# Kernel optimization log

Measured on AMD Instinct MI355X. Metric: run time of the kernel, lower is better.

## Reference

```python
import jax, jax.numpy as jnp
import numpy as np

B, N, DIM, HEADS, DHEAD, DEPTH, EDGE = 1, 384, 128, 4, 64, 3, 8
INNER = HEADS * DHEAD  # 256


def _make_rotary():
    inv = 1.0 / (10000.0 ** (np.arange(0, DHEAD, 2, dtype=np.float32) / DHEAD))
    f = np.arange(N, dtype=np.float32)[:, None] * inv[None, :]  # [N, DHEAD//2]
    f = np.repeat(f, 2, axis=-1)  # interleaved pairs -> [N, DHEAD]
    return jnp.asarray(np.cos(f)), jnp.asarray(np.sin(f))

COS, SIN = _make_rotary()


def _rotate_half(x):
    x2 = x.reshape(x.shape[:-1] + (DHEAD // 2, 2))
    return jnp.stack((-x2[..., 1], x2[..., 0]), axis=-1).reshape(x.shape)


def _layer_norm(x, s, b, eps=1e-3):
    mu = jnp.mean(x, axis=-1, keepdims=True)
    var = jnp.mean(jnp.square(x - mu), axis=-1, keepdims=True)
    return (x - mu) * jax.lax.rsqrt(var + eps) * s + b


def _gated_res(x, res, Wg):
    gi = jnp.concatenate([x, res, x - res], axis=-1)  # [B,N,3*DIM]
    g = jax.nn.sigmoid(gi @ Wg)  # [B,N,1]
    return x * g + res * (1.0 - g)


def setup_inputs() -> dict:
    key = jax.random.key(0)
    ks = jax.random.split(key, 16)
    p = lambda k, shape: 0.02 * jax.random.normal(k, shape, jnp.float32)
    return {
        "nodes": jax.random.normal(ks[0], (B, N, DIM), jnp.float32),
        "edges": jax.random.normal(ks[1], (B, N, N, EDGE), jnp.float32),
        "ln1_s": jnp.ones((DEPTH, DIM), jnp.float32), "ln1_b": jnp.zeros((DEPTH, DIM), jnp.float32),
        "Wq": p(ks[2], (DEPTH, DIM, INNER)), "bq": jnp.zeros((DEPTH, INNER), jnp.float32),
        "Wkv": p(ks[3], (DEPTH, DIM, 2 * INNER)), "bkv": jnp.zeros((DEPTH, 2 * INNER), jnp.float32),
        "We": p(ks[4], (DEPTH, EDGE, INNER)), "be": jnp.zeros((DEPTH, INNER), jnp.float32),
        "Wo": p(ks[5], (DEPTH, INNER, DIM)), "bo": jnp.zeros((DEPTH, DIM), jnp.float32),
        "Wg_attn": p(ks[6], (DEPTH, 3 * DIM, 1)),
        "ln2_s": jnp.ones((DEPTH, DIM), jnp.float32), "ln2_b": jnp.zeros((DEPTH, DIM), jnp.float32),
        "W1": p(ks[7], (DEPTH, DIM, 4 * DIM)), "b1": jnp.zeros((DEPTH, 4 * DIM), jnp.float32),
        "W2": p(ks[8], (DEPTH, 4 * DIM, DIM)), "b2": jnp.zeros((DEPTH, DIM), jnp.float32),
        "Wg_ff": p(ks[9], (DEPTH, 3 * DIM, 1)),
        "Wd1": p(ks[10], (DIM, 9)), "bd1": jnp.zeros((9,), jnp.float32),
        "Wd2": p(ks[11], (9, 3)), "bd2": jnp.zeros((3,), jnp.float32),
        "mask": jnp.ones((B, N), dtype=bool),
    }


def _forward(nodes, edges, ln1_s, ln1_b, Wq, bq, Wkv, bkv, We, be, Wo, bo, Wg_attn,
             ln2_s, ln2_b, W1, b1, W2, b2, Wg_ff, Wd1, bd1, Wd2, bd2, mask):
    cos = COS[None, None]  # [1,1,N,DHEAD]
    sin = SIN[None, None]
    mask2 = mask[:, None, :, None] & mask[:, None, None, :]  # [B,1,N,N]
    x = nodes
    for i in range(DEPTH):
        # --- pre-norm attention with edge-conditioned K/V and rotary pos emb ---
        xn = _layer_norm(x, ln1_s[i], ln1_b[i])
        q = (xn @ Wq[i] + bq[i]).reshape(B, N, HEADS, DHEAD).transpose(0, 2, 1, 3)
        k, v = jnp.split(xn @ Wkv[i] + bkv[i], 2, axis=-1)
        k = k.reshape(B, N, HEADS, DHEAD).transpose(0, 2, 1, 3)
        v = v.reshape(B, N, HEADS, DHEAD).transpose(0, 2, 1, 3)
        e = (edges @ We[i] + be[i]).reshape(B, N, N, HEADS, DHEAD).transpose(0, 3, 1, 2, 4)  # [B,H,i,j,d]
        q = q * cos + _rotate_half(q) * sin
        k = k * cos + _rotate_half(k) * sin
        kf = k[:, :, None, :, :] + e  # [B,H,i,j,d]
        vf = v[:, :, None, :, :] + e
        sim = jnp.einsum('bhid,bhijd->bhij', q, kf) * (DHEAD ** -0.5)
        sim = jnp.where(mask2, sim, -1e9)
        attn = jax.nn.softmax(sim, axis=-1)
        out = jnp.einsum('bhij,bhijd->bhid', attn, vf)
        out = out.transpose(0, 2, 1, 3).reshape(B, N, INNER) @ Wo[i] + bo[i]
        x = _gated_res(out, x, Wg_attn[i])
        # --- pre-norm feedforward ---
        xn2 = _layer_norm(x, ln2_s[i], ln2_b[i])
        h = jax.nn.gelu(xn2 @ W1[i] + b1[i], approximate=False)
        ff = h @ W2[i] + b2[i]
        x = _gated_res(ff, x, Wg_ff[i])
    y = jax.nn.relu(x @ Wd1 + bd1)
    y = y @ Wd2 + bd2  # [B,N,3]
    return y - jnp.mean(y, axis=1)  # broadcasts since B == 1 (matches TF semantics)


def reference(nodes, edges, ln1_s, ln1_b, Wq, bq, Wkv, bkv, We, be, Wo, bo, Wg_attn,
              ln2_s, ln2_b, W1, b1, W2, b2, Wg_ff, Wd1, bd1, Wd2, bd2, mask):
    return _forward(nodes, edges, ln1_s, ln1_b, Wq, bq, Wkv, bkv, We, be, Wo, bo, Wg_attn,
                    ln2_s, ln2_b, W1, b1, W2, b2, Wg_ff, Wd1, bd1, Wd2, bd2, mask)
```

## Files before the change

kernel.cpp:

```cpp
#include <hip/hip_runtime.h>
#include <math.h>

#define NTOK 384
#define DIM  128
#define HEADS 4
#define DHEAD 64
#define INNER 256
#define DEPTH 3
#define EDGE 8
#define FFD 512

__device__ __forceinline__ float wave_sum64(float v){
#pragma unroll
  for (int m = 32; m >= 1; m >>= 1) v += __shfl_xor(v, m, 64);
  return v;
}
__device__ __forceinline__ float wave_max64(float v){
#pragma unroll
  for (int m = 32; m >= 1; m >>= 1) v = fmaxf(v, __shfl_xor(v, m, 64));
  return v;
}

__device__ __forceinline__ int swz_row(int id){ return (id & 7) * 48 + (id >> 3); }

__device__ __forceinline__ void rotary_val(int i, int d, float* c, float* s){
  int j = d >> 1;
  double ex = (double)(2 * j) / 64.0;
  float p = (float)pow(10000.0, ex);
  float inv = 1.0f / p;
  float f = (float)i * inv;
  double fd = (double)f;
  *c = (float)cos(fd);
  *s = (float)sin(fd);
}

__device__ __forceinline__ void qkv_row_512(
    int i, int t, const float* __restrict__ snx,
    const float* __restrict__ Wq, const float* __restrict__ bq,
    const float* __restrict__ Wkv, const float* __restrict__ bkv,
    const float* __restrict__ We, const float* __restrict__ be,
    const float* __restrict__ cosRow, const float* __restrict__ sinRow,
    float* __restrict__ qb_, float* __restrict__ kbT, float* __restrict__ vb_,
    float* __restrict__ qWeB, float* __restrict__ qbeB)
{
  if (t >= 384) return;
  const float2* Wp; const float* bb; int pcol; int stride;
  if (t < 128)      { Wp = (const float2*)Wq + t;              stride = 128; bb = bq;        pcol = t; }
  else if (t < 256) { Wp = (const float2*)Wkv + (t - 128);     stride = 256; bb = bkv;       pcol = t - 128; }
  else              { Wp = (const float2*)Wkv + 128 + (t - 256); stride = 256; bb = bkv + 256; pcol = t - 256; }

  float a0 = 0.f, a1 = 0.f;
#pragma unroll 8
  for (int k = 0; k < 128; ++k){
    float2 w = Wp[(size_t)k * stride];
    float xr = snx[k];
    a0 = fmaf(xr, w.x, a0); a1 = fmaf(xr, w.y, a1);
  }
  a0 += bb[2 * pcol]; a1 += bb[2 * pcol + 1];

  if (t < 256){
    int dloc = (2 * pcol) & 63;
    float c = cosRow[dloc], s = sinRow[dloc];
    float r0 = a0 * c - a1 * s;
    float r1 = a1 * c + a0 * s;
    if (t < 128){
      qb_[i * 256 + 2 * pcol]     = r0;
      qb_[i * 256 + 2 * pcol + 1] = r1;
      int h = pcol >> 5;
#pragma unroll
      for (int cc = 0; cc < 8; ++cc){
        float pr = r0 * We[cc * 256 + 2 * pcol] + r1 * We[cc * 256 + 2 * pcol + 1];
#pragma unroll
        for (int m = 16; m >= 1; m >>= 1) pr += __shfl_xor(pr, m, 32);
        if ((t & 31) == 0) qWeB[(h * NTOK + i) * 8 + cc] = pr;
      }
      float pb = r0 * be[2 * pcol] + r1 * be[2 * pcol + 1];
#pragma unroll
      for (int m = 16; m >= 1; m >>= 1) pb += __shfl_xor(pb, m, 32);
      if ((t & 31) == 0) qbeB[h * NTOK + i] = pb;
    } else {
      int h = pcol >> 5, d0 = 2 * (pcol & 31);
      kbT[(size_t)(h * 64 + d0) * NTOK + i]     = r0;
      kbT[(size_t)(h * 64 + d0 + 1) * NTOK + i] = r1;
    }
  } else {
    vb_[i * 256 + 2 * pcol]     = a0;
    vb_[i * 256 + 2 * pcol + 1] = a1;
  }
}

__global__ __launch_bounds__(512) void k_lnqkv(
    const float* __restrict__ x,
    const float* __restrict__ ls, const float* __restrict__ lb,
    const float* __restrict__ Wq, const float* __restrict__ bq,
    const float* __restrict__ Wkv, const float* __restrict__ bkv,
    const float* __restrict__ We, const float* __restrict__ be,
    float* __restrict__ cosS, float* __restrict__ sinS,
    float* __restrict__ qb_, float* __restrict__ kbT, float* __restrict__ vb_,
    float* __restrict__ qWeB, float* __restrict__ qbeB)
{
  __shared__ float snx[128];
  __shared__ float crow[64], srow[64];
  __shared__ float red[4];
  int i = swz_row(blockIdx.x);
  int t = threadIdx.x;

  if (t >= 448){
    int d = t - 448;
    float c, s;
    rotary_val(i, d, &c, &s);
    crow[d] = c; srow[d] = s;
    cosS[i * 64 + d] = c; sinS[i * 64 + d] = s;
  }
  float xv = (t < 128) ? x[(size_t)i * 128 + t] : 0.f;
  float s = (t < 128) ? wave_sum64(xv) : 0.f;
  if (t == 0)  red[0] = s;
  if (t == 64) red[1] = s;
  __syncthreads();
  float mu = (red[0] + red[1]) * (1.0f / 128.0f);
  float d = xv - mu;
  float s2 = (t < 128) ? wave_sum64(d * d) : 0.f;
  if (t == 0)  red[2] = s2;
  if (t == 64) red[3] = s2;
  __syncthreads();
  if (t < 128){
    float var = (red[2] + red[3]) * (1.0f / 128.0f);
    float rstd = 1.0f / sqrtf(var + 1e-3f);
    snx[t] = d * rstd * ls[t] + lb[t];
  }
  __syncthreads();
  qkv_row_512(i, t, snx, Wq, bq, Wkv, bkv, We, be, crow, srow,
              qb_, kbT, vb_, qWeB, qbeB);
}

__global__ __launch_bounds__(384) void k_attn(
    const float* __restrict__ qb_, const float* __restrict__ kbT, const float* __restrict__ vb_,
    const float* __restrict__ qWeB, const float* __restrict__ qbeB,
    const float* __restrict__ edges,
    const float* __restrict__ We, const float* __restrict__ be,
    float* __restrict__ aout)
{
  __shared__ float qs[64];
  __shared__ float qw[8];
  __shared__ float qbs_s;
  __shared__ float attnL[NTOK];
  __shared__ float redA[6], redB[6];
  __shared__ float red8[6][8];
  __shared__ float aws[8];
  __shared__ float part[NTOK];

  int id = blockIdx.x;
  int xcd = id & 7, loc = id >> 3;
  int i = xcd * 48 + (loc % 48);
  int h = loc / 48;
  int t = threadIdx.x, lane = t & 63, wv = t >> 6;

  if (t < 64) qs[t] = qb_[i * 256 + h * 64 + t];
  else if (t < 72) qw[t - 64] = qWeB[(h * NTOK + i) * 8 + (t - 64)];
  else if (t == 72) qbs_s = qbeB[h * NTOK + i];
  __syncthreads();

  const float* kTp = kbT + (size_t)(h * 64) * NTOK + t;
  float ac0 = 0.f, ac1 = 0.f, ac2 = 0.f, ac3 = 0.f;
#pragma unroll 8
  for (int d = 0; d < 64; d += 4){
    ac0 = fmaf(qs[d],     kTp[(size_t)d * NTOK],       ac0);
    ac1 = fmaf(qs[d + 1], kTp[(size_t)(d + 1) * NTOK], ac1);
    ac2 = fmaf(qs[d + 2], kTp[(size_t)(d + 2) * NTOK], ac2);
    ac3 = fmaf(qs[d + 3], kTp[(size_t)(d + 3) * NTOK], ac3);
  }
  const float* ep = edges + ((size_t)i * NTOK + t) * 8;
  float4 e0 = *(const float4*)ep;
  float4 e1 = *(const float4*)(ep + 4);
  float ed = e0.x * qw[0] + e0.y * qw[1] + e0.z * qw[2] + e0.w * qw[3]
           + e1.x * qw[4] + e1.y * qw[5] + e1.z * qw[6] + e1.w * qw[7];
  float sim = 0.125f * (ac0 + ac1 + ac2 + ac3 + ed + qbs_s);

  float mx = wave_max64(sim);
  if (lane == 0) redA[wv] = mx;
  __syncthreads();
  float gm = fmaxf(fmaxf(fmaxf(redA[0], redA[1]), fmaxf(redA[2], redA[3])),
                   fmaxf(redA[4], redA[5]));
  float e = expf(sim - gm);
  float sm = wave_sum64(e);
  if (lane == 0) redB[wv] = sm;
  __syncthreads();
  float tot = redB[0] + redB[1] + redB[2] + redB[3] + redB[4] + redB[5];
  float w = e / tot;
  attnL[t] = w;

  float a8[8] = { w * e0.x, w * e0.y, w * e0.z, w * e0.w,
                  w * e1.x, w * e1.y, w * e1.z, w * e1.w };
#pragma unroll
  for (int cc = 0; cc < 8; ++cc){
    float r = wave_sum64(a8[cc]);
    if (lane == 0) red8[wv][cc] = r;
  }
  __syncthreads();
  if (t < 8){
    float sa = 0.f;
#pragma unroll
    for (int g = 0; g < 6; ++g) sa += red8[g][t];
    aws[t] = sa;
  }
  __syncthreads();

  {
    int dd = lane;
    const float* vp = vb_ + h * 64 + dd;
    int j0 = wv * 64;
    float va = 0.f, vb2 = 0.f;
#pragma unroll 8
    for (int jj = 0; jj < 64; jj += 2){
      va  = fmaf(attnL[j0 + jj],     vp[(size_t)(j0 + jj) * 256],     va);
      vb2 = fmaf(attnL[j0 + jj + 1], vp[(size_t)(j0 + jj + 1) * 256], vb2);
    }
    part[t] = va + vb2;
  }
  __syncthreads();
  if (t < 64){
    float o = part[t] + part[64 + t] + part[128 + t] + part[192 + t]
            + part[256 + t] + part[320 + t];
    float ew = 0.f;
#pragma unroll
    for (int cc = 0; cc < 8; ++cc) ew = fmaf(aws[cc], We[cc * 256 + h * 64 + t], ew);
    o += ew + be[h * 64 + t];
    aout[i * 256 + h * 64 + t] = o;
  }
}

__global__ __launch_bounds__(512) void k_tail(
    const float* __restrict__ aout,
    const float* __restrict__ Wo, const float* __restrict__ bo,
    const float* __restrict__ Wg_a,
    const float* __restrict__ ln2s, const float* __restrict__ ln2b,
    const float* __restrict__ W1, const float* __restrict__ b1,
    const float* __restrict__ W2, const float* __restrict__ b2,
    const float* __restrict__ Wg_f,
    const float* __restrict__ xin, float* __restrict__ xout,
    int has_next,
    const float* __restrict__ ls_n, const float* __restrict__ lb_n,
    const float* __restrict__ Wq_n, const float* __restrict__ bq_n,
    const float* __restrict__ Wkv_n, const float* __restrict__ bkv_n,
    const float* __restrict__ We_n, const float* __restrict__ be_n,
    const float* __restrict__ cosS, const float* __restrict__ sinS,
    float* __restrict__ qb_, float* __restrict__ kbT, float* __restrict__ vb_,
    float* __restrict__ qWeB, float* __restrict__ qbeB)
{
  __shared__ float ar[256];
  __shared__ float xold[128];
  __shared__ float xrow[128];
  __shared__ float snx[128];
  __shared__ float hs[512];
  __shared__ float4 prL[512];
  __shared__ float red[4];
  float* prF = (float*)prL;

  int i = swz_row(blockIdx.x);
  int t = threadIdx.x;

  if (t < 64)            ((float4*)ar)[t]        = ((const float4*)(aout + (size_t)i * 256))[t];
  else if (t < 96)       ((float4*)xold)[t - 64] = ((const float4*)(xin + (size_t)i * 128))[t - 64];
  __syncthreads();

  {
    int colq = t & 31, ksub = t >> 5;
    const float4* Wo4 = (const float4*)Wo;
    float4 acc = {0.f, 0.f, 0.f, 0.f};
#pragma unroll
    for (int kk = 0; kk < 16; ++kk){
      int k = ksub * 16 + kk;
      float4 w = Wo4[(size_t)k * 32 + colq];
      float a = ar[k];
      acc.x = fmaf(a, w.x, acc.x); acc.y = fmaf(a, w.y, acc.y);
      acc.z = fmaf(a, w.z, acc.z); acc.w = fmaf(a, w.w, acc.w);
    }
    prL[ksub * 32 + colq] = acc;
  }
  __syncthreads();

  float o = 0.f;
  if (t < 128){
    o = bo[t];
#pragma unroll
    for (int s = 0; s < 16; ++s) o += prF[s * 128 + t];
    float xo = xold[t];
    float gp = o * Wg_a[t] + xo * Wg_a[128 + t] + (o - xo) * Wg_a[256 + t];
    float sg = wave_sum64(gp);
    if (t == 0)  red[0] = sg;
    if (t == 64) red[1] = sg;
  }
  __syncthreads();
  if (t < 128){
    float z = red[0] + red[1];
    float gg = 1.0f / (1.0f + expf(-z));
    xrow[t] = o * gg + xold[t] * (1.0f - gg);
  }
  __syncthreads();
  float xv2 = (t < 128) ? xrow[t] : 0.f;
  float s = (t < 128) ? wave_sum64(xv2) : 0.f;
  if (t == 0)  red[0] = s;
  if (t == 64) red[1] = s;
  __syncthreads();
  float mu = (red[0] + red[1]) * (1.0f / 128.0f);
  float dcen = xv2 - mu;
  float s2 = (t < 128) ? wave_sum64(dcen * dcen) : 0.f;
  if (t == 0)  red[2] = s2;
  if (t == 64) red[3] = s2;
  __syncthreads();
  if (t < 128){
    float var = (red[2] + red[3]) * (1.0f / 128.0f);
    float rstd = 1.0f / sqrtf(var + 1e-3f);
    snx[t] = dcen * rstd * ln2s[t] + ln2b[t];
  }
  __syncthreads();

  {
    int colq = t & 127, ksub = t >> 7;
    const float4* W14 = (const float4*)W1;
    float4 acc = {0.f, 0.f, 0.f, 0.f};
#pragma unroll 8
    for (int kk = 0; kk < 32; ++kk){
      int k = ksub * 32 + kk;
      float4 w = W14[(size_t)k * 128 + colq];
      float a = snx[k];
      acc.x = fmaf(a, w.x, acc.x); acc.y = fmaf(a, w.y, acc.y);
      acc.z = fmaf(a, w.z, acc.z); acc.w = fmaf(a, w.w, acc.w);
    }
    prL[ksub * 128 + colq] = acc;
  }
  __syncthreads();

  {
    float h = b1[t];
#pragma unroll
    for (int s3 = 0; s3 < 4; ++s3) h += prF[s3 * 512 + t];
    const float RS2 = 0.70710678118654752440f;
    hs[t] = 0.5f * h * (1.0f + erff(h * RS2));
  }
  __syncthreads();

  {
    int colq = t & 31, ksub = t >> 5;
    const float4* W24 = (const float4*)W2;
    float4 acc = {0.f, 0.f, 0.f, 0.f};
#pragma unroll 8
    for (int kk = 0; kk < 32; ++kk){
      int k = ksub * 32 + kk;
      float4 w = W24[(size_t)k * 32 + colq];
      float a = hs[k];
      acc.x = fmaf(a, w.x, acc.x); acc.y = fmaf(a, w.y, acc.y);
      acc.z = fmaf(a, w.z, acc.z); acc.w = fmaf(a, w.w, acc.w);
    }
    prL[ksub * 32 + colq] = acc;
  }
  __syncthreads();

  float f = 0.f;
  if (t < 128){
    f = b2[t];
#pragma unroll
    for (int s3 = 0; s3 < 16; ++s3) f += prF[s3 * 128 + t];
    float xr = xrow[t];
    float gp = f * Wg_f[t] + xr * Wg_f[128 + t] + (f - xr) * Wg_f[256 + t];
    float sg = wave_sum64(gp);
    if (t == 0)  red[0] = sg;
    if (t == 64) red[1] = sg;
  }
  __syncthreads();
  float xnew = 0.f;
  if (t < 128){
    float z = red[0] + red[1];
    float gg = 1.0f / (1.0f + expf(-z));
    xnew = f * gg + xrow[t] * (1.0f - gg);
    xout[(size_t)i * 128 + t] = xnew;
  }
  if (has_next){
    float sn = (t < 128) ? wave_sum64(xnew) : 0.f;
    if (t == 0)  red[0] = sn;
    if (t == 64) red[1] = sn;
    __syncthreads();
    float mun = (red[0] + red[1]) * (1.0f / 128.0f);
    float dn = xnew - mun;
    float sn2 = (t < 128) ? wave_sum64(dn * dn) : 0.f;
    if (t == 0)  red[2] = sn2;
    if (t == 64) red[3] = sn2;
    __syncthreads();
    if (t < 128){
      float var = (red[2] + red[3]) * (1.0f / 128.0f);
      float rstd = 1.0f / sqrtf(var + 1e-3f);
      snx[t] = dn * rstd * ls_n[t] + lb_n[t];
    }
    __syncthreads();
    qkv_row_512(i, t, snx, Wq_n, bq_n, Wkv_n, bkv_n, We_n, be_n,
                cosS + (size_t)i * 64, sinS + (size_t)i * 64,
                qb_, kbT, vb_, qWeB, qbeB);
  }
}

__global__ __launch_bounds__(384) void k_final(
    const float* __restrict__ x,
    const float* __restrict__ Wd1, const float* __restrict__ bd1,
    const float* __restrict__ Wd2, const float* __restrict__ bd2,
    float* __restrict__ out)
{
  __shared__ float red[6];
  int i = threadIdx.x;
  float y[9];
#pragma unroll
  for (int c = 0; c < 9; ++c) y[c] = bd1[c];
  const float4* x4 = (const float4*)(x + (size_t)i * 128);
#pragma unroll 8
  for (int r4 = 0; r4 < 32; ++r4){
    float4 xv = x4[r4];
    const float* wp = Wd1 + (r4 * 4) * 9;
#pragma unroll
    for (int c = 0; c < 9; ++c) y[c] = fmaf(xv.x, wp[c], y[c]);
#pragma unroll
    for (int c = 0; c < 9; ++c) y[c] = fmaf(xv.y, wp[9 + c], y[c]);
#pragma unroll
    for (int c = 0; c < 9; ++c) y[c] = fmaf(xv.z, wp[18 + c], y[c]);
#pragma unroll
    for (int c = 0; c < 9; ++c) y[c] = fmaf(xv.w, wp[27 + c], y[c]);
  }
#pragma unroll
  for (int c = 0; c < 9; ++c) y[c] = fmaxf(y[c], 0.0f);
  float z[3];
#pragma unroll
  for (int c = 0; c < 3; ++c){
    float a = bd2[c];
#pragma unroll
    for (int r = 0; r < 9; ++r) a = fmaf(y[r], Wd2[r * 3 + c], a);
    z[c] = a;
  }
#pragma unroll
  for (int c = 0; c < 3; ++c){
    float s = wave_sum64(z[c]);
    if ((i & 63) == 0) red[i >> 6] = s;
    __syncthreads();
    float tot = 0.f;
#pragma unroll
    for (int w = 0; w < 6; ++w) tot += red[w];
    float mean = tot * (1.0f / 384.0f);
    out[i * 3 + c] = z[c] - mean;
    __syncthreads();
  }
}

extern "C" void kernel_launch(void* const* d_in, const int* in_sizes, int n_in,
                              void* d_out, int out_size, void* d_ws, size_t ws_size,
                              hipStream_t stream)
{
  const float* nodes   = (const float*)d_in[0];
  const float* edges   = (const float*)d_in[1];
  const float* ln1_s   = (const float*)d_in[2];
  const float* ln1_b   = (const float*)d_in[3];
  const float* Wq      = (const float*)d_in[4];
  const float* bq      = (const float*)d_in[5];
  const float* Wkv     = (const float*)d_in[6];
  const float* bkv     = (const float*)d_in[7];
  const float* We      = (const float*)d_in[8];
  const float* be      = (const float*)d_in[9];
  const float* Wo      = (const float*)d_in[10];
  const float* bo      = (const float*)d_in[11];
  const float* Wg_attn = (const float*)d_in[12];
  const float* ln2_s   = (const float*)d_in[13];
  const float* ln2_b   = (const float*)d_in[14];
  const float* W1      = (const float*)d_in[15];
  const float* b1      = (const float*)d_in[16];
  const float* W2      = (const float*)d_in[17];
  const float* b2      = (const float*)d_in[18];
  const float* Wg_ff   = (const float*)d_in[19];
  const float* Wd1     = (const float*)d_in[20];
  const float* bd1     = (const float*)d_in[21];
  const float* Wd2     = (const float*)d_in[22];
  const float* bd2     = (const float*)d_in[23];

  float* ws   = (float*)d_ws;
  float* cosS = ws;
  float* sinS = cosS + 24576;
  float* qbuf = sinS + 24576;
  float* kbT  = qbuf + 98304;
  float* vbuf = kbT + 98304;
  float* qWeB = vbuf + 98304;
  float* qbeB = qWeB + 12288;
  float* aoutB = qbeB + 1536;
  float* xbuf = aoutB + 98304;

  k_lnqkv<<<dim3(NTOK), dim3(512), 0, stream>>>(
      nodes, ln1_s, ln1_b, Wq, bq, Wkv, bkv, We, be,
      cosS, sinS, qbuf, kbT, vbuf, qWeB, qbeB);

  for (int L = 0; L < DEPTH; ++L){
    int Ln = (L < DEPTH - 1) ? (L + 1) : L;
    k_attn<<<dim3(NTOK * HEADS), dim3(384), 0, stream>>>(
        qbuf, kbT, vbuf, qWeB, qbeB, edges,
        We + (size_t)L * EDGE * INNER, be + L * INNER, aoutB);
    k_tail<<<dim3(NTOK), dim3(512), 0, stream>>>(
        aoutB, Wo + (size_t)L * INNER * DIM, bo + L * DIM,
        Wg_attn + L * 3 * DIM,
        ln2_s + L * DIM, ln2_b + L * DIM,
        W1 + (size_t)L * DIM * FFD, b1 + L * FFD,
        W2 + (size_t)L * FFD * DIM, b2 + L * DIM,
        Wg_ff + L * 3 * DIM,
        (L == 0) ? nodes : xbuf, xbuf,
        (L < DEPTH - 1) ? 1 : 0,
        ln1_s + Ln * DIM, ln1_b + Ln * DIM,
        Wq + (size_t)Ln * DIM * INNER, bq + Ln * INNER,
        Wkv + (size_t)Ln * DIM * 2 * INNER, bkv + Ln * 2 * INNER,
        We + (size_t)Ln * EDGE * INNER, be + Ln * INNER,
        cosS, sinS, qbuf, kbT, vbuf, qWeB, qbeB);
  }

  k_final<<<dim3(1), dim3(384), 0, stream>>>(xbuf, Wd1, bd1, Wd2, bd2, (float*)d_out);
}
```

Measured before the change: 153.9 us.

## Split fused tail kernel into projection, FFN and QKV kernels with more blocks

Replaces the single per-row tail kernel, which ran one 512-thread block per token, with four smaller kernels: output projection plus gate plus LN2, FFN1 split over two column halves, FFN2 split over two column halves, and the next layer's QKV split into three parts. The aim is to raise the block count and parallelism so more CUs are busy during the serial per-row GEMVs. The cost is extra launches and global round trips for intermediate buffers. The gate and layernorm work is also recomputed in each of the three QKV blocks.

```diff
diff --git a/kernel.cpp b/kernel.cpp
--- a/kernel.cpp
+++ b/kernel.cpp
@@ -229,63 +229,202 @@
   }
 }
 
-__global__ __launch_bounds__(512) void k_tail(
+__global__ __launch_bounds__(256) void k_projgate(
     const float* __restrict__ aout,
     const float* __restrict__ Wo, const float* __restrict__ bo,
     const float* __restrict__ Wg_a,
     const float* __restrict__ ln2s, const float* __restrict__ ln2b,
+    const float* __restrict__ xin,
+    float* __restrict__ snx2buf, float* __restrict__ xrowB)
+{
+  __shared__ float ain[256];
+  __shared__ float xo[128];
+  __shared__ float orow[128];
+  __shared__ float xrow[128];
+  __shared__ float4 pr[256];
+  __shared__ float red[4];
+
+  int i = swz_row(blockIdx.x);
+  int t = threadIdx.x;
+
+  ain[t] = aout[(size_t)i * 256 + t];
+  if (t < 128) xo[t] = xin[(size_t)i * 128 + t];
+  __syncthreads();
+
+  {
+    int cq = t & 31, ks = t >> 5;
+    const float4* Wo4 = (const float4*)Wo;
+    float4 acc = {0.f, 0.f, 0.f, 0.f};
+#pragma unroll
+    for (int kk = 0; kk < 32; ++kk){
+      int k = ks * 32 + kk;
+      float4 w = Wo4[(size_t)k * 32 + cq];
+      float a = ain[k];
+      acc.x = fmaf(a, w.x, acc.x); acc.y = fmaf(a, w.y, acc.y);
+      acc.z = fmaf(a, w.z, acc.z); acc.w = fmaf(a, w.w, acc.w);
+    }
+    pr[ks * 32 + cq] = acc;
+  }
+  __syncthreads();
+  if (t < 32){
+    float4 s = pr[t];
+#pragma unroll
+    for (int s3 = 1; s3 < 8; ++s3){
+      float4 p = pr[s3 * 32 + t];
+      s.x += p.x; s.y += p.y; s.z += p.z; s.w += p.w;
+    }
+    float4 b = ((const float4*)bo)[t];
+    s.x += b.x; s.y += b.y; s.z += b.z; s.w += b.w;
+    ((float4*)orow)[t] = s;
+  }
+  __syncthreads();
+
+  if (t < 128){
+    float o = orow[t], xov = xo[t];
+    float gp = o * Wg_a[t] + xov * Wg_a[128 + t] + (o - xov) * Wg_a[256 + t];
+    float sg = wave_sum64(gp);
+    if (t == 0)  red[0] = sg;
+    if (t == 64) red[1] = sg;
+  }
+  __syncthreads();
+  if (t < 128){
+    float z = red[0] + red[1];
+    float gg = 1.0f / (1.0f + expf(-z));
+    float xr = orow[t] * gg + xo[t] * (1.0f - gg);
+    xrow[t] = xr;
+    xrowB[(size_t)i * 128 + t] = xr;
+    float s = wave_sum64(xr);
+    if (t == 0)  red[2] = s;
+    if (t == 64) red[3] = s;
+  }
+  __syncthreads();
+  if (t < 128){
+    float mu = (red[2] + red[3]) * (1.0f / 128.0f);
+    float dc = xrow[t] - mu;
+    float s2 = wave_sum64(dc * dc);
+    if (t == 0)  red[0] = s2;
+    if (t == 64) red[1] = s2;
+    __syncthreads();
+    float var = (red[0] + red[1]) * (1.0f / 128.0f);
+    float rstd = 1.0f / sqrtf(var + 1e-3f);
+    snx2buf[(size_t)i * 128 + t] = dc * rstd * ln2s[t] + ln2b[t];
+  } else {
+    __syncthreads();
+  }
+}
+
+__global__ __launch_bounds__(256) void k_ffn1(
+    const float* __restrict__ snx2buf,
     const float* __restrict__ W1, const float* __restrict__ b1,
+    float* __restrict__ hbuf)
+{
+  __shared__ float sx[128];
+  __shared__ float2 pr2[128];
+  int id = blockIdx.x;
+  int xcd = id & 7, loc = id >> 3;
+  int i = xcd * 48 + (loc >> 1);
+  int ch = loc & 1;
+  int t = threadIdx.x;
+
+  if (t < 128) sx[t] = snx2buf[(size_t)i * 128 + t];
+  __syncthreads();
+
+  int cp = t & 127, ks = t >> 7;
+  int c2 = ch * 128 + cp;
+  const float2* W12 = (const float2*)W1;
+  float a0 = 0.f, a1 = 0.f;
+#pragma unroll 8
+  for (int kk = 0; kk < 64; ++kk){
+    int k = ks * 64 + kk;
+    float2 w = W12[(size_t)k * 256 + c2];
+    float x = sx[k];
+    a0 = fmaf(x, w.x, a0); a1 = fmaf(x, w.y, a1);
+  }
+  if (ks == 1){ pr2[cp].x = a0; pr2[cp].y = a1; }
+  __syncthreads();
+  if (ks == 0){
+    a0 += pr2[cp].x + b1[2 * c2];
+    a1 += pr2[cp].y + b1[2 * c2 + 1];
+    const float RS2 = 0.70710678118654752440f;
+    float g0 = 0.5f * a0 * (1.0f + erff(a0 * RS2));
+    float g1 = 0.5f * a1 * (1.0f + erff(a1 * RS2));
+    float2 gv; gv.x = g0; gv.y = g1;
+    ((float2*)hbuf)[(size_t)i * 256 + c2] = gv;
+  }
+}
+
+__global__ __launch_bounds__(256) void k_ffn2(
+    const float* __restrict__ hbuf,
     const float* __restrict__ W2, const float* __restrict__ b2,
+    float* __restrict__ fbuf)
+{
+  __shared__ float hh[512];
+  __shared__ float4 pr[256];
+  int id = blockIdx.x;
+  int xcd = id & 7, loc = id >> 3;
+  int i = xcd * 48 + (loc >> 1);
+  int hc = loc & 1;
+  int t = threadIdx.x;
+
+  hh[t] = hbuf[(size_t)i * 512 + t];
+  hh[256 + t] = hbuf[(size_t)i * 512 + 256 + t];
+  __syncthreads();
+
+  int q = t & 15, ks = t >> 4;
+  int gq = hc * 16 + q;
+  const float4* W24 = (const float4*)W2;
+  float4 acc = {0.f, 0.f, 0.f, 0.f};
+#pragma unroll
+  for (int kk = 0; kk < 32; ++kk){
+    int k = ks * 32 + kk;
+    float4 w = W24[(size_t)k * 32 + gq];
+    float a = hh[k];
+    acc.x = fmaf(a, w.x, acc.x); acc.y = fmaf(a, w.y, acc.y);
+    acc.z = fmaf(a, w.z, acc.z); acc.w = fmaf(a, w.w, acc.w);
+  }
+  pr[ks * 16 + q] = acc;
+  __syncthreads();
+  if (t < 16){
+    float4 s = pr[t];
+#pragma unroll
+    for (int s3 = 1; s3 < 16; ++s3){
+      float4 p = pr[s3 * 16 + t];
+      s.x += p.x; s.y += p.y; s.z += p.z; s.w += p.w;
+    }
+    float4 b = ((const float4*)b2)[gq];
+    s.x += b.x; s.y += b.y; s.z += b.z; s.w += b.w;
+    ((float4*)fbuf)[(size_t)i * 32 + gq] = s;
+  }
+}
+
+__global__ __launch_bounds__(256) void k_qkv(
+    const float* __restrict__ fbuf, const float* __restrict__ xrowB,
     const float* __restrict__ Wg_f,
-    const float* __restrict__ xin, float* __restrict__ xout,
-    int has_next,
     const float* __restrict__ ls_n, const float* __restrict__ lb_n,
     const float* __restrict__ Wq_n, const float* __restrict__ bq_n,
     const float* __restrict__ Wkv_n, const float* __restrict__ bkv_n,
     const float* __restrict__ We_n, const float* __restrict__ be_n,
     const float* __restrict__ cosS, const float* __restrict__ sinS,
+    float* __restrict__ xbuf,
     float* __restrict__ qb_, float* __restrict__ kbT, float* __restrict__ vb_,
     float* __restrict__ qWeB, float* __restrict__ qbeB)
 {
-  __shared__ float ar[256];
-  __shared__ float xold[128];
-  __shared__ float xrow[128];
   __shared__ float snx[128];
-  __shared__ float hs[512];
-  __shared__ float4 prL[512];
+  __shared__ float xnewL[128];
+  __shared__ float2 qp2[128];
   __shared__ float red[4];
-  float* prF = (float*)prL;
-
-  int i = swz_row(blockIdx.x);
+
+  int id = blockIdx.x;
+  int xcd = id & 7, loc = id >> 3;
+  int i = xcd * 48 + loc / 3;
+  int part = loc % 3;
   int t = threadIdx.x;
 
-  if (t < 64)            ((float4*)ar)[t]        = ((const float4*)(aout + (size_t)i * 256))[t];
-  else if (t < 96)       ((float4*)xold)[t - 64] = ((const float4*)(xin + (size_t)i * 128))[t - 64];
-  __syncthreads();
-
-  {
-    int colq = t & 31, ksub = t >> 5;
-    const float4* Wo4 = (const float4*)Wo;
-    float4 acc = {0.f, 0.f, 0.f, 0.f};
-#pragma unroll
-    for (int kk = 0; kk < 16; ++kk){
-      int k = ksub * 16 + kk;
-      float4 w = Wo4[(size_t)k * 32 + colq];
-      float a = ar[k];
-      acc.x = fmaf(a, w.x, acc.x); acc.y = fmaf(a, w.y, acc.y);
-      acc.z = fmaf(a, w.z, acc.z); acc.w = fmaf(a, w.w, acc.w);
-    }
-    prL[ksub * 32 + colq] = acc;
-  }
-  __syncthreads();
-
-  float o = 0.f;
+  float fv = 0.f, xr = 0.f;
   if (t < 128){
-    o = bo[t];
-#pragma unroll
-    for (int s = 0; s < 16; ++s) o += prF[s * 128 + t];
-    float xo = xold[t];
-    float gp = o * Wg_a[t] + xo * Wg_a[128 + t] + (o - xo) * Wg_a[256 + t];
+    fv = fbuf[(size_t)i * 128 + t];
+    xr = xrowB[(size_t)i * 128 + t];
+    float gp = fv * Wg_f[t] + xr * Wg_f[128 + t] + (fv - xr) * Wg_f[256 + t];
     float sg = wave_sum64(gp);
     if (t == 0)  red[0] = sg;
     if (t == 64) red[1] = sg;
@@ -294,108 +433,97 @@
   if (t < 128){
     float z = red[0] + red[1];
     float gg = 1.0f / (1.0f + expf(-z));
-    xrow[t] = o * gg + xold[t] * (1.0f - gg);
-  }
-  __syncthreads();
-  float xv2 = (t < 128) ? xrow[t] : 0.f;
-  float s = (t < 128) ? wave_sum64(xv2) : 0.f;
-  if (t == 0)  red[0] = s;
-  if (t == 64) red[1] = s;
-  __syncthreads();
-  float mu = (red[0] + red[1]) * (1.0f / 128.0f);
-  float dcen = xv2 - mu;
-  float s2 = (t < 128) ? wave_sum64(dcen * dcen) : 0.f;
-  if (t == 0)  red[2] = s2;
-  if (t == 64) red[3] = s2;
+    float xn = fv * gg + xr * (1.0f - gg);
+    xnewL[t] = xn;
+    if (part == 0) xbuf[(size_t)i * 128 + t] = xn;
+    float s = wave_sum64(xn);
+    if (t == 0)  red[2] = s;
+    if (t == 64) red[3] = s;
+  }
   __syncthreads();
   if (t < 128){
-    float var = (red[2] + red[3]) * (1.0f / 128.0f);
+    float mu = (red[2] + red[3]) * (1.0f / 128.0f);
+    float dn = xnewL[t] - mu;
+    float s2 = wave_sum64(dn * dn);
+    if (t == 0)  red[0] = s2;
+    if (t == 64) red[1] = s2;
+    __syncthreads();
+    float var = (red[0] + red[1]) * (1.0f / 128.0f);
     float rstd = 1.0f / sqrtf(var + 1e-3f);
-    snx[t] = dcen * rstd * ln2s[t] + ln2b[t];
-  }
-  __syncthreads();
-
-  {
-    int colq = t & 127, ksub = t >> 7;
-    const float4* W14 = (const float4*)W1;
-    float4 acc = {0.f, 0.f, 0.f, 0.f};
+    snx[t] = dn * rstd * ls_n[t] + lb_n[t];
+  } else {
+    __syncthreads();
+  }
+  __syncthreads();
+
+  int cp = t & 127, ks = t >> 7;
+  const float2* Wp; const float* bb; int stride;
+  if (part == 0)      { Wp = (const float2*)Wq_n + cp;        stride = 128; bb = bq_n; }
+  else if (part == 1) { Wp = (const float2*)Wkv_n + cp;       stride = 256; bb = bkv_n; }
+  else                { Wp = (const float2*)Wkv_n + 128 + cp; stride = 256; bb = bkv_n + 256; }
+
+  float a0 = 0.f, a1 = 0.f;
 #pragma unroll 8
-    for (int kk = 0; kk < 32; ++kk){
-      int k = ksub * 32 + kk;
-      float4 w = W14[(size_t)k * 128 + colq];
-      float a = snx[k];
-      acc.x = fmaf(a, w.x, acc.x); acc.y = fmaf(a, w.y, acc.y);
-      acc.z = fmaf(a, w.z, acc.z); acc.w = fmaf(a, w.w, acc.w);
+  for (int kk = 0; kk < 64; ++kk){
+    int k = ks * 64 + kk;
+    float2 w = Wp[(size_t)k * stride];
+    float x = snx[k];
+    a0 = fmaf(x, w.x, a0); a1 = fmaf(x, w.y, a1);
+  }
+  if (ks == 1){ qp2[cp].x = a0; qp2[cp].y = a1; }
+  __syncthreads();
+  if (ks == 0){
+    a0 += qp2[cp].x + bb[2 * cp];
+    a1 += qp2[cp].y + bb[2 * cp + 1];
+    if (part < 2){
+      int dloc = (2 * cp) & 63;
+      float c = cosS[i * 64 + dloc], s = sinS[i * 64 + dloc];
+      float r0 = a0 * c - a1 * s;
+      float r1 = a1 * c + a0 * s;
+      if (part == 0){
+        qb_[i * 256 + 2 * cp]     = r0;
+        qb_[i * 256 + 2 * cp + 1] = r1;
+        int h = cp >> 5;
+#pragma unroll
+        for (int cc = 0; cc < 8; ++cc){
+          float pr = r0 * We_n[cc * 256 + 2 * cp] + r1 * We_n[cc * 256 + 2 * cp + 1];
+#pragma unroll
+          for (int m = 16; m >= 1; m >>= 1) pr += __shfl_xor(pr, m, 32);
+          if ((t & 31) == 0) qWeB[(h * NTOK + i) * 8 + cc] = pr;
+        }
+        float pb = r0 * be_n[2 * cp] + r1 * be_n[2 * cp + 1];
+#pragma unroll
+        for (int m = 16; m >= 1; m >>= 1) pb += __shfl_xor(pb, m, 32);
+        if ((t & 31) == 0) qbeB[h * NTOK + i] = pb;
+      } else {
+        int h = cp >> 5, d0 = 2 * (cp & 31);
+        kbT[(size_t)(h * 64 + d0) * NTOK + i]     = r0;
+        kbT[(size_t)(h * 64 + d0 + 1) * NTOK + i] = r1;
+      }
+    } else {
+      vb_[i * 256 + 2 * cp]     = a0;
+      vb_[i * 256 + 2 * cp + 1] = a1;
     }
-    prL[ksub * 128 + colq] = acc;
-  }
-  __syncthreads();
-
-  {
-    float h = b1[t];
-#pragma unroll
-    for (int s3 = 0; s3 < 4; ++s3) h += prF[s3 * 512 + t];
-    const float RS2 = 0.70710678118654752440f;
-    hs[t] = 0.5f * h * (1.0f + erff(h * RS2));
-  }
-  __syncthreads();
-
-  {
-    int colq = t & 31, ksub = t >> 5;
-    const float4* W24 = (const float4*)W2;
-    float4 acc = {0.f, 0.f, 0.f, 0.f};
-#pragma unroll 8
-    for (int kk = 0; kk < 32; ++kk){
-      int k = ksub * 32 + kk;
-      float4 w = W24[(size_t)k * 32 + colq];
-      float a = hs[k];
-      acc.x = fmaf(a, w.x, acc.x); acc.y = fmaf(a, w.y, acc.y);
-      acc.z = fmaf(a, w.z, acc.z); acc.w = fmaf(a, w.w, acc.w);
-    }
-    prL[ksub * 32 + colq] = acc;
-  }
-  __syncthreads();
-
-  float f = 0.f;
-  if (t < 128){
-    f = b2[t];
-#pragma unroll
-    for (int s3 = 0; s3 < 16; ++s3) f += prF[s3 * 128 + t];
-    float xr = xrow[t];
-    float gp = f * Wg_f[t] + xr * Wg_f[128 + t] + (f - xr) * Wg_f[256 + t];
-    float sg = wave_sum64(gp);
-    if (t == 0)  red[0] = sg;
-    if (t == 64) red[1] = sg;
-  }
-  __syncthreads();
-  float xnew = 0.f;
-  if (t < 128){
-    float z = red[0] + red[1];
-    float gg = 1.0f / (1.0f + expf(-z));
-    xnew = f * gg + xrow[t] * (1.0f - gg);
-    xout[(size_t)i * 128 + t] = xnew;
-  }
-  if (has_next){
-    float sn = (t < 128) ? wave_sum64(xnew) : 0.f;
-    if (t == 0)  red[0] = sn;
-    if (t == 64) red[1] = sn;
-    __syncthreads();
-    float mun = (red[0] + red[1]) * (1.0f / 128.0f);
-    float dn = xnew - mun;
-    float sn2 = (t < 128) ? wave_sum64(dn * dn) : 0.f;
-    if (t == 0)  red[2] = sn2;
-    if (t == 64) red[3] = sn2;
-    __syncthreads();
-    if (t < 128){
-      float var = (red[2] + red[3]) * (1.0f / 128.0f);
-      float rstd = 1.0f / sqrtf(var + 1e-3f);
-      snx[t] = dn * rstd * ls_n[t] + lb_n[t];
-    }
-    __syncthreads();
-    qkv_row_512(i, t, snx, Wq_n, bq_n, Wkv_n, bkv_n, We_n, be_n,
-                cosS + (size_t)i * 64, sinS + (size_t)i * 64,
-                qb_, kbT, vb_, qWeB, qbeB);
-  }
+  }
+}
+
+__global__ __launch_bounds__(128) void k_gatelast(
+    const float* __restrict__ fbuf, const float* __restrict__ xrowB,
+    const float* __restrict__ Wg_f, float* __restrict__ xbuf)
+{
+  __shared__ float red[2];
+  int i = swz_row(blockIdx.x);
+  int t = threadIdx.x;
+  float fv = fbuf[(size_t)i * 128 + t];
+  float xr = xrowB[(size_t)i * 128 + t];
+  float gp = fv * Wg_f[t] + xr * Wg_f[128 + t] + (fv - xr) * Wg_f[256 + t];
+  float sg = wave_sum64(gp);
+  if (t == 0)  red[0] = sg;
+  if (t == 64) red[1] = sg;
+  __syncthreads();
+  float z = red[0] + red[1];
+  float gg = 1.0f / (1.0f + expf(-z));
+  xbuf[(size_t)i * 128 + t] = fv * gg + xr * (1.0f - gg);
 }
 
 __global__ __launch_bounds__(384) void k_final(
@@ -476,40 +604,50 @@
   const float* Wd2     = (const float*)d_in[22];
   const float* bd2     = (const float*)d_in[23];
 
-  float* ws   = (float*)d_ws;
-  float* cosS = ws;
-  float* sinS = cosS + 24576;
-  float* qbuf = sinS + 24576;
-  float* kbT  = qbuf + 98304;
-  float* vbuf = kbT + 98304;
-  float* qWeB = vbuf + 98304;
-  float* qbeB = qWeB + 12288;
+  float* ws    = (float*)d_ws;
+  float* cosS  = ws;
+  float* sinS  = cosS + 24576;
+  float* qbuf  = sinS + 24576;
+  float* kbT   = qbuf + 98304;
+  float* vbuf  = kbT + 98304;
+  float* qWeB  = vbuf + 98304;
+  float* qbeB  = qWeB + 12288;
   float* aoutB = qbeB + 1536;
-  float* xbuf = aoutB + 98304;
+  float* xbuf  = aoutB + 98304;
+  float* snx2B = xbuf + 49152;
+  float* xrowB = snx2B + 49152;
+  float* fbuf  = xrowB + 49152;
+  float* hbuf  = fbuf + 49152;
 
   k_lnqkv<<<dim3(NTOK), dim3(512), 0, stream>>>(
       nodes, ln1_s, ln1_b, Wq, bq, Wkv, bkv, We, be,
       cosS, sinS, qbuf, kbT, vbuf, qWeB, qbeB);
 
   for (int L = 0; L < DEPTH; ++L){
-    int Ln = (L < DEPTH - 1) ? (L + 1) : L;
     k_attn<<<dim3(NTOK * HEADS), dim3(384), 0, stream>>>(
         qbuf, kbT, vbuf, qWeB, qbeB, edges,
         We + (size_t)L * EDGE * INNER, be + L * INNER, aoutB);
-    k_tail<<<dim3(NTOK), dim3(512), 0, stream>>>(
+    k_projgate<<<dim3(NTOK), dim3(256), 0, stream>>>(
         aoutB, Wo + (size_t)L * INNER * DIM, bo + L * DIM,
-        Wg_attn + L * 3 * DIM,
-        ln2_s + L * DIM, ln2_b + L * DIM,
-        W1 + (size_t)L * DIM * FFD, b1 + L * FFD,
-        W2 + (size_t)L * FFD * DIM, b2 + L * DIM,
-        Wg_ff + L * 3 * DIM,
-        (L == 0) ? nodes : xbuf, xbuf,
-        (L < DEPTH - 1) ? 1 : 0,
-        ln1_s + Ln * DIM, ln1_b + Ln * DIM,
-        Wq + (size_t)Ln * DIM * INNER, bq + Ln * INNER,
-        Wkv + (size_t)Ln * DIM * 2 * INNER, bkv + Ln * 2 * INNER,
-        We + (size_t)Ln * EDGE * INNER, be + Ln * INNER,
-        cosS, sinS, qbuf, kbT, vbuf, qWeB, qbeB);
+        Wg_attn + L * 3 * DIM, ln2_s + L * DIM, ln2_b + L * DIM,
+        (L == 0) ? nodes : xbuf, snx2B, xrowB);
+    k_ffn1<<<dim3(NTOK * 2), dim3(256), 0, stream>>>(
+        snx2B, W1 + (size_t)L * DIM * FFD, b1 + L * FFD, hbuf);
+    k_ffn2<<<dim3(NTOK * 2), dim3(256), 0, stream>>>(
+        hbuf, W2 + (size_t)L * FFD * DIM, b2 + L * DIM, fbuf);
+    if (L < DEPTH - 1){
+      int Ln = L + 1;
+      k_qkv<<<dim3(NTOK * 3), dim3(256), 0, stream>>>(
+          fbuf, xrowB, Wg_ff + L * 3 * DIM,
+          ln1_s + Ln * DIM, ln1_b + Ln * DIM,
+          Wq + (size_t)Ln * DIM * INNER, bq + Ln * INNER,
+          Wkv + (size_t)Ln * DIM * 2 * INNER, bkv + Ln * 2 * INNER,
+          We + (size_t)Ln * EDGE * INNER, be + Ln * INNER,
+          cosS, sinS, xbuf, qbuf, kbT, vbuf, qWeB, qbeB);
+    } else {
+      k_gatelast<<<dim3(NTOK), dim3(128), 0, stream>>>(
+          fbuf, xrowB, Wg_ff + L * 3 * DIM, xbuf);
+    }
   }
 
   k_final<<<dim3(1), dim3(384), 0, stream>>>(xbuf, Wd1, bd1, Wd2, bd2, (float*)d_out);
```

Measured after the change: 174.1 us. 13.1% more time.
